# Kernel optimization log

Hardware: AMD Instinct MI355X
Metric: run time of the kernel (lower is better)

Reference implementation:

```python
import jax, jax.numpy as jnp
import numpy as np

EPS_ROW = 1e-8
EPS_BN = 1e-5


def _row_norm(A):
    # A / clamp(rowsum, 1e-8)
    return A / jnp.clip(A.sum(axis=1, keepdims=True), EPS_ROW, None)


def _bn_eval(x, gamma, beta, mean, var):
    return (x - mean) * (gamma / jnp.sqrt(var + EPS_BN)) + beta


def setup_inputs() -> dict:
    key = jax.random.key(0)
    ks = jax.random.split(key, 12)
    n_src, n_tgt = 8192, 16384
    d_src, d_tgt_in, d_hid, d_out = 256, 128, 128, 64

    def xavier(k, fan_in, fan_out):
        lim = float(np.sqrt(6.0 / (fan_in + fan_out)))
        # stored as [in, out] so forward is x @ W + b
        return jax.random.uniform(k, (fan_in, fan_out), jnp.float32, -lim, lim)

    inp = {
        "H_source": jax.random.normal(ks[0], (n_src, d_src), jnp.float32),
        "H_target": jax.random.normal(ks[1], (n_tgt, d_tgt_in), jnp.float32),
        "A": jax.random.uniform(ks[2], (n_tgt, n_src), jnp.float32),
        "W0": xavier(ks[3], d_src, d_hid),
        "b0": jnp.zeros((d_hid,), jnp.float32),
        "Wb0": xavier(ks[4], d_hid, d_hid),
        "bb0": jnp.zeros((d_hid,), jnp.float32),
        "W1": xavier(ks[5], d_hid, d_hid),
        "b1": jnp.zeros((d_hid,), jnp.float32),
        # fwd BN layers (i=0 and i=2): stacked [2, d_hid]
        "bn_f_gamma": jax.random.uniform(ks[6], (2, d_hid), jnp.float32, 0.5, 1.5),
        "bn_f_beta": jax.random.normal(ks[7], (2, d_hid), jnp.float32) * 0.1,
        "bn_f_mean": jax.random.normal(ks[8], (2, d_hid), jnp.float32) * 0.1,
        "bn_f_var": jax.random.uniform(ks[9], (2, d_hid), jnp.float32, 0.5, 1.5),
        # bwd BN layer (i=1)
        "bn_b_gamma": jax.random.uniform(ks[10], (d_hid,), jnp.float32, 0.5, 1.5),
        "bn_b_beta": jnp.zeros((d_hid,), jnp.float32),
        "bn_b_mean": jnp.zeros((d_hid,), jnp.float32),
        "bn_b_var": jnp.ones((d_hid,), jnp.float32),
        "Wout": xavier(ks[11], d_hid, d_out),
        "bout": jnp.zeros((d_out,), jnp.float32),
    }
    return inp


def reference(H_source, H_target, A, W0, b0, Wb0, bb0, W1, b1,
              bn_f_gamma, bn_f_beta, bn_f_mean, bn_f_var,
              bn_b_gamma, bn_b_beta, bn_b_mean, bn_b_var,
              Wout, bout):
    # Inference mode: dropout = identity, BatchNorm uses running stats.
    A_n = _row_norm(A)          # [n_tgt, n_src]
    AT_n = _row_norm(A.T)       # [n_src, n_tgt]

    # layer 0 (fwd): target <- source
    h_tgt = (A_n @ H_source) @ W0 + b0
    h_tgt = jax.nn.relu(_bn_eval(h_tgt, bn_f_gamma[0], bn_f_beta[0], bn_f_mean[0], bn_f_var[0]))

    # layer 1 (bwd): source <- target
    h_src = (AT_n @ h_tgt) @ Wb0 + bb0
    h_src = jax.nn.relu(_bn_eval(h_src, bn_b_gamma, bn_b_beta, bn_b_mean, bn_b_var))

    # layer 2 (fwd): target <- source
    h_tgt = (A_n @ h_src) @ W1 + b1
    h_tgt = jax.nn.relu(_bn_eval(h_tgt, bn_f_gamma[1], bn_f_beta[1], bn_f_mean[1], bn_f_var[1]))

    return h_tgt @ Wout + bout  # [n_tgt, d_out]
```

## Files before the change

### kernel.cpp

```cpp
#include <hip/hip_runtime.h>
#include <hip/hip_bf16.h>
#include <stdint.h>

typedef unsigned short ushort_t;
typedef float   f32x4  __attribute__((ext_vector_type(4)));
typedef short   bf16x8 __attribute__((ext_vector_type(8)));

#define NSRC 8192
#define NTGT 16384

__device__ __forceinline__ ushort_t f2bf(float f){
  union { float f; uint32_t u; } v; v.f = f;
  uint32_t r = v.u + 0x7fffu + ((v.u >> 16) & 1u);
  return (ushort_t)(r >> 16);
}
__device__ __forceinline__ uint2 pack4(f32x4 v){
  uint2 r;
  r.x = (uint32_t)f2bf(v.x) | ((uint32_t)f2bf(v.y) << 16);
  r.y = (uint32_t)f2bf(v.z) | ((uint32_t)f2bf(v.w) << 16);
  return r;
}
__device__ __forceinline__ bf16x8 cvt8(f32x4 lo, f32x4 hi){
  union { uint4 u; bf16x8 h; } x;
  uint2 a = pack4(lo), b = pack4(hi);
  x.u = make_uint4(a.x, a.y, b.x, b.y);
  return x.h;
}
__device__ __forceinline__ uint4 asu4(bf16x8 v){ union { bf16x8 h; uint4 u; } x; x.h = v; return x.u; }
__device__ __forceinline__ float sum4(f32x4 v){ return v.x + v.y + v.z + v.w; }

typedef __attribute__((address_space(1))) const uint32_t* gas_t;
typedef __attribute__((address_space(3))) uint32_t* las_t;
__device__ __forceinline__ void dma16(const void* g, void* l){
  __builtin_amdgcn_global_load_lds((gas_t)g, (las_t)l, 16, 0, 0);
}

__global__ __launch_bounds__(256) void k_wt(const float* __restrict__ S, ushort_t* __restrict__ D,
                                            int R, int C){
  __shared__ float tile[32][33];
  const int cb = blockIdx.x * 32, rb = blockIdx.y * 32;
  const int tx = threadIdx.x & 31, ty = threadIdx.x >> 5;
#pragma unroll
  for (int i = 0; i < 4; ++i)
    tile[ty + 8*i][tx] = S[(size_t)(rb + ty + 8*i) * C + cb + tx];
  __syncthreads();
#pragma unroll
  for (int i = 0; i < 4; ++i)
    D[(size_t)(cb + ty + 8*i) * R + rb + tx] = f2bf(tile[tx][ty + 8*i]);
}

__global__ __launch_bounds__(256) void k_packH(const float* __restrict__ S, ushort_t* __restrict__ D){
  int u = blockIdx.x * 4 + (threadIdx.x >> 6);
  int lane = threadIdx.x & 63;
  int nb = u >> 8, kb = u & 255;
  int fr = lane & 15, q = lane >> 4;
  ushort_t buf[8];
#pragma unroll
  for (int j = 0; j < 8; ++j)
    buf[j] = f2bf(S[(size_t)(kb * 32 + q * 8 + j) * 256 + nb * 16 + fr]);
  *(uint4*)&D[((size_t)nb * 256 + kb) * 512 + (size_t)lane * 8] = *(uint4*)buf;
}

__global__ void k_init_b2p_tail(ushort_t* __restrict__ B2p){
  int idx = blockIdx.x * 256 + threadIdx.x;
  int lane = idx & 63;
  int kb = idx >> 6;
  int fr = lane & 15;
  uint32_t v = (fr == 0) ? 0x3F803F80u : 0u;
  uint4 val = {v, v, v, v};
  *(uint4*)&B2p[((size_t)8 * 512 + kb) * 512 + (size_t)lane * 8] = val;
}

__global__ __launch_bounds__(256) void k_gemm1(const float* __restrict__ A,
    const ushort_t* __restrict__ B1p, float* __restrict__ P2, float* __restrict__ rowsumP,
    ushort_t* __restrict__ Abf){
  __shared__ ushort_t Bls[2][16 * 512];
  const int t = threadIdx.x;
  const int mb = blockIdx.x, kc = blockIdx.y;
  const size_t m0 = (size_t)mb * 64;
  const int k0 = kc * 2048;
  const int kb0 = k0 >> 5;

  const int w = t >> 6, lane = t & 63;
  const int wr = w >> 1, wc = w & 1;
  const int fr = lane & 15, q = lane >> 4;

  const float* pa0 = &A[(m0 + wr * 32 + fr) * (size_t)NSRC + k0 + q * 8];
  const float* pa1 = pa0 + (size_t)16 * NSRC;
  ushort_t* pw0 = &Abf[(m0 + wr * 32 + fr) * (size_t)NSRC + k0 + q * 8];
  ushort_t* pw1 = pw0 + (size_t)16 * NSRC;

#pragma unroll
  for (int i = 0; i < 4; ++i){
    int f = w * 4 + i;
    dma16(&B1p[((size_t)f * 256 + kb0) * 512 + (size_t)lane * 8], &Bls[0][f * 512]);
  }
  f32x4 c0a = *(const f32x4*)pa0, c0b = *(const f32x4*)(pa0 + 4);
  f32x4 c1a = *(const f32x4*)pa1, c1b = *(const f32x4*)(pa1 + 4);

  f32x4 acc[2][8];
  const f32x4 vz = {0.f, 0.f, 0.f, 0.f};
#pragma unroll
  for (int i = 0; i < 2; ++i)
#pragma unroll
    for (int j = 0; j < 8; ++j) acc[i][j] = vz;
  float rs0 = 0.f, rs1 = 0.f;
  __syncthreads();

  for (int kt = 0; kt < 64; ++kt){
    const int cur = kt & 1;
    f32x4 n0a, n0b, n1a, n1b;
    if (kt < 63){
#pragma unroll
      for (int i = 0; i < 4; ++i){
        int f = w * 4 + i;
        dma16(&B1p[((size_t)f * 256 + kb0 + kt + 1) * 512 + (size_t)lane * 8],
              &Bls[cur ^ 1][f * 512]);
      }
      n0a = *(const f32x4*)(pa0 + (kt + 1) * 32);
      n0b = *(const f32x4*)(pa0 + (kt + 1) * 32 + 4);
      n1a = *(const f32x4*)(pa1 + (kt + 1) * 32);
      n1b = *(const f32x4*)(pa1 + (kt + 1) * 32 + 4);
    }

    rs0 += sum4(c0a) + sum4(c0b);
    rs1 += sum4(c1a) + sum4(c1b);
    bf16x8 af0 = cvt8(c0a, c0b);
    bf16x8 af1 = cvt8(c1a, c1b);
    if (wc == 0){
      *(uint4*)&pw0[kt * 32] = asu4(af0);
      *(uint4*)&pw1[kt * 32] = asu4(af1);
    }
#pragma unroll
    for (int fn = 0; fn < 8; ++fn){
      bf16x8 bfv = *(bf16x8*)&Bls[cur][(wc * 8 + fn) * 512 + lane * 8];
      acc[0][fn] = __builtin_amdgcn_mfma_f32_16x16x32_bf16(af0, bfv, acc[0][fn], 0, 0, 0);
      acc[1][fn] = __builtin_amdgcn_mfma_f32_16x16x32_bf16(af1, bfv, acc[1][fn], 0, 0, 0);
    }
    if (kt < 63){ c0a = n0a; c0b = n0b; c1a = n1a; c1b = n1b; }
    __syncthreads();
  }

  float* Pd = P2 + (size_t)kc * NTGT * 256;
#pragma unroll
  for (int fm = 0; fm < 2; ++fm)
#pragma unroll
    for (int j = 0; j < 4; ++j){
      int row = wr * 32 + fm * 16 + q * 4 + j;
#pragma unroll
      for (int fn = 0; fn < 8; ++fn)
        Pd[(m0 + row) * 256 + wc * 128 + fn * 16 + fr] = acc[fm][fn][j];
    }

  rs0 += __shfl_xor(rs0, 16); rs0 += __shfl_xor(rs0, 32);
  rs1 += __shfl_xor(rs1, 16); rs1 += __shfl_xor(rs1, 32);
  if (wc == 0 && q == 0){
    rowsumP[(size_t)kc * NTGT + m0 + wr * 32 + fr]      = rs0;
    rowsumP[(size_t)kc * NTGT + m0 + wr * 32 + 16 + fr] = rs1;
  }
}

__global__ __launch_bounds__(256) void k_gemm2(const ushort_t* __restrict__ Abf,
    const ushort_t* __restrict__ B2p, float* __restrict__ G2p){
  __shared__ ushort_t Bls[2][9 * 512];
  const int t = threadIdx.x;
  const int sb = blockIdx.x, kc = blockIdx.y;
  const size_t s0 = (size_t)sb * 64;
  const int k0 = kc * 2048;
  const int kb0 = k0 >> 5;

  const int w = t >> 6, lane = t & 63;
  const int fr = lane & 15, q = lane >> 4;
  const size_t scol = s0 + w * 16 + fr;
  const ushort_t* pA = &Abf[(size_t)(k0 + q * 8) * NSRC + scol];

  const int f0 = w * 3;
  const int nf = (w < 3) ? 3 : 0;

#pragma unroll
  for (int i = 0; i < 3; ++i){
    if (i < nf)
      dma16(&B2p[((size_t)(f0 + i) * 512 + kb0) * 512 + (size_t)lane * 8], &Bls[0][(f0 + i) * 512]);
  }
  ushort_t arc[8];
#pragma unroll
  for (int j = 0; j < 8; ++j)
    arc[j] = pA[(size_t)j * NSRC];

  f32x4 acc[9];
  const f32x4 vz = {0.f, 0.f, 0.f, 0.f};
#pragma unroll
  for (int j = 0; j < 9; ++j) acc[j] = vz;
  __syncthreads();

  for (int kt = 0; kt < 64; ++kt){
    const int cur = kt & 1;
    ushort_t arn[8];
    if (kt < 63){
#pragma unroll
      for (int i = 0; i < 3; ++i){
        if (i < nf)
          dma16(&B2p[((size_t)(f0 + i) * 512 + kb0 + kt + 1) * 512 + (size_t)lane * 8],
                &Bls[cur ^ 1][(f0 + i) * 512]);
      }
#pragma unroll
      for (int j = 0; j < 8; ++j)
        arn[j] = pA[((size_t)(kt + 1) * 32 + j) * NSRC];
    }

    bf16x8 af;
#pragma unroll
    for (int j = 0; j < 8; ++j) af[j] = (short)arc[j];
#pragma unroll
    for (int fn = 0; fn < 9; ++fn){
      bf16x8 bfv = *(bf16x8*)&Bls[cur][fn * 512 + lane * 8];
      acc[fn] = __builtin_amdgcn_mfma_f32_16x16x32_bf16(af, bfv, acc[fn], 0, 0, 0);
    }
    if (kt < 63){
#pragma unroll
      for (int j = 0; j < 8; ++j) arc[j] = arn[j];
    }
    __syncthreads();
  }

  float* Pd = G2p + (size_t)kc * NSRC * 144;
#pragma unroll
  for (int j = 0; j < 4; ++j){
    int row = w * 16 + q * 4 + j;
#pragma unroll
    for (int fn = 0; fn < 9; ++fn)
      Pd[(s0 + row) * 144 + fn * 16 + fr] = acc[fn][j];
  }
}

__global__ __launch_bounds__(256) void k_gemm3(const ushort_t* __restrict__ Abf,
    const ushort_t* __restrict__ B3p, float* __restrict__ G3p){
  __shared__ ushort_t Bls[2][8 * 512];
  const int t = threadIdx.x;
  const int mb = blockIdx.x, kc = blockIdx.y;
  const size_t m0 = (size_t)mb * 64;
  const int k0 = kc * 2048;
  const int kb0 = k0 >> 5;

  const int w = t >> 6, lane = t & 63;
  const int wr = w >> 1, wc = w & 1;
  const int fr = lane & 15, q = lane >> 4;

  const ushort_t* pa0 = &Abf[(m0 + wr * 32 + fr) * (size_t)NSRC + k0 + q * 8];
  const ushort_t* pa1 = pa0 + (size_t)16 * NSRC;

#pragma unroll
  for (int i = 0; i < 2; ++i){
    int f = w * 2 + i;
    dma16(&B3p[((size_t)f * 256 + kb0) * 512 + (size_t)lane * 8], &Bls[0][f * 512]);
  }
  bf16x8 a0c = *(const bf16x8*)pa0;
  bf16x8 a1c = *(const bf16x8*)pa1;

  f32x4 acc[2][4];
  const f32x4 vz = {0.f, 0.f, 0.f, 0.f};
#pragma unroll
  for (int i = 0; i < 2; ++i)
#pragma unroll
    for (int j = 0; j < 4; ++j) acc[i][j] = vz;
  __syncthreads();

  for (int kt = 0; kt < 64; ++kt){
    const int cur = kt & 1;
    bf16x8 a0n, a1n;
    if (kt < 63){
#pragma unroll
      for (int i = 0; i < 2; ++i){
        int f = w * 2 + i;
        dma16(&B3p[((size_t)f * 256 + kb0 + kt + 1) * 512 + (size_t)lane * 8],
              &Bls[cur ^ 1][f * 512]);
      }
      a0n = *(const bf16x8*)(pa0 + (kt + 1) * 32);
      a1n = *(const bf16x8*)(pa1 + (kt + 1) * 32);
    }

#pragma unroll
    for (int fn = 0; fn < 4; ++fn){
      bf16x8 bfv = *(bf16x8*)&Bls[cur][(wc * 4 + fn) * 512 + lane * 8];
      acc[0][fn] = __builtin_amdgcn_mfma_f32_16x16x32_bf16(a0c, bfv, acc[0][fn], 0, 0, 0);
      acc[1][fn] = __builtin_amdgcn_mfma_f32_16x16x32_bf16(a1c, bfv, acc[1][fn], 0, 0, 0);
    }
    if (kt < 63){ a0c = a0n; a1c = a1n; }
    __syncthreads();
  }

  float* Pd = G3p + (size_t)kc * NTGT * 128;
#pragma unroll
  for (int fm = 0; fm < 2; ++fm)
#pragma unroll
    for (int j = 0; j < 4; ++j){
      int row = wr * 32 + fm * 16 + q * 4 + j;
#pragma unroll
      for (int fn = 0; fn < 4; ++fn)
        Pd[(m0 + row) * 128 + wc * 64 + fn * 16 + fr] = acc[fm][fn][j];
    }
}

__global__ __launch_bounds__(256) void k_s1(
    const float* __restrict__ P2, const float* __restrict__ rowsumP,
    const ushort_t* __restrict__ W0t, const float* __restrict__ b0,
    const float* __restrict__ g, const float* __restrict__ be,
    const float* __restrict__ mu, const float* __restrict__ va,
    ushort_t* __restrict__ B2p)
{
  __shared__ ushort_t Xs[64 * 72];
  __shared__ ushort_t Ws[128 * 72];
  __shared__ float    os[64 * 132];
  __shared__ float invs[64], scs[128], mbs[128];
  const int t = threadIdx.x;
  const size_t m0 = (size_t)blockIdx.x * 64;
  const size_t CH = (size_t)NTGT * 256;

  if (t < 64){
    float rsv = rowsumP[m0 + t] + rowsumP[(size_t)NTGT + m0 + t]
              + rowsumP[2 * (size_t)NTGT + m0 + t] + rowsumP[3 * (size_t)NTGT + m0 + t];
    invs[t] = 1.0f / fmaxf(rsv, 1e-8f);
  } else if (t < 192){
    int n = t - 64;
    float s = g[n] * rsqrtf(va[n] + 1e-5f);
    scs[n] = s;
    mbs[n] = (b0[n] - mu[n]) * s + be[n];
  }
  __syncthreads();

  const int w = t >> 6, lane = t & 63;
  const int wr = w >> 1, wc = w & 1;
  const int fr = lane & 15, q = lane >> 4;
  f32x4 acc[2][4];
  const f32x4 vz = {0.f, 0.f, 0.f, 0.f};
#pragma unroll
  for (int i = 0; i < 2; ++i)
#pragma unroll
    for (int j = 0; j < 4; ++j) acc[i][j] = vz;

  for (int kt = 0; kt < 4; ++kt){
    const int kk = kt * 64;
    __syncthreads();
#pragma unroll
    for (int r = 0; r < 4; ++r){
      int c = t + 256 * r;
      int row = c >> 4, col4 = (c & 15) * 4;
      const float* pa = &P2[(m0 + row) * 256 + kk + col4];
      f32x4 v0 = *(const f32x4*)pa;
      f32x4 v1 = *(const f32x4*)(pa + CH);
      f32x4 v2 = *(const f32x4*)(pa + 2 * CH);
      f32x4 v3 = *(const f32x4*)(pa + 3 * CH);
      f32x4 v = (v0 + v1 + v2 + v3) * invs[row];
      *(uint2*)&Xs[row * 72 + col4] = pack4(v);
    }
#pragma unroll
    for (int r = 0; r < 4; ++r){
      int c = t + 256 * r;
      int n = c >> 3, k8 = (c & 7) * 8;
      *(uint4*)&Ws[n * 72 + k8] = *(const uint4*)&W0t[(size_t)n * 256 + kk + k8];
    }
    __syncthreads();
#pragma unroll
    for (int ks = 0; ks < 2; ++ks){
      bf16x8 af[2], bfv[4];
      af[0] = *(const bf16x8*)&Xs[(wr * 32 + fr) * 72 + ks * 32 + q * 8];
      af[1] = *(const bf16x8*)&Xs[(wr * 32 + 16 + fr) * 72 + ks * 32 + q * 8];
#pragma unroll
      for (int fn = 0; fn < 4; ++fn)
        bfv[fn] = *(const bf16x8*)&Ws[(wc * 64 + fn * 16 + fr) * 72 + ks * 32 + q * 8];
#pragma unroll
      for (int fm = 0; fm < 2; ++fm)
#pragma unroll
        for (int fn = 0; fn < 4; ++fn)
          acc[fm][fn] = __builtin_amdgcn_mfma_f32_16x16x32_bf16(af[fm], bfv[fn], acc[fm][fn], 0, 0, 0);
    }
  }

#pragma unroll
  for (int fm = 0; fm < 2; ++fm)
#pragma unroll
    for (int fn = 0; fn < 4; ++fn){
      int n = wc * 64 + fn * 16 + fr;
      float s = scs[n], mb = mbs[n];
#pragma unroll
      for (int j = 0; j < 4; ++j){
        int row = wr * 32 + fm * 16 + q * 4 + j;
        os[row * 132 + n] = fmaxf(acc[fm][fn][j] * s + mb, 0.f);
      }
    }
  __syncthreads();
  {
    const int kb0 = (int)(m0 >> 5);
#pragma unroll
    for (int r = 0; r < 4; ++r){
      int s = t + 256 * r;
      int lane2 = s & 63;
      int kb2 = (s >> 6) & 1;
      int nb = s >> 7;
      int fr2 = lane2 & 15, q2 = lane2 >> 4;
      int n = nb * 16 + fr2;
      ushort_t buf[8];
#pragma unroll
      for (int j = 0; j < 8; ++j)
        buf[j] = f2bf(os[(kb2 * 32 + q2 * 8 + j) * 132 + n]);
      *(uint4*)&B2p[((size_t)nb * 512 + kb0 + kb2) * 512 + (size_t)lane2 * 8] = *(uint4*)buf;
    }
  }
}

__global__ __launch_bounds__(256) void k_s2(
    const float* __restrict__ G2p,
    const ushort_t* __restrict__ Wb0t, const float* __restrict__ bb0,
    const float* __restrict__ g, const float* __restrict__ be,
    const float* __restrict__ mu, const float* __restrict__ va,
    ushort_t* __restrict__ B3p)
{
  __shared__ ushort_t Xs[64 * 72];
  __shared__ ushort_t Ws[128 * 72];
  __shared__ float    os[64 * 132];
  __shared__ float invs[64], scs[128], mbs[128];
  const int t = threadIdx.x;
  const size_t m0 = (size_t)blockIdx.x * 64;
  const size_t CH = (size_t)NSRC * 144;

  if (t < 64){
    size_t row = m0 + t;
    float c = 0.f;
#pragma unroll
    for (int i = 0; i < 8; ++i) c += G2p[i * CH + row * 144 + 128];
    invs[t] = 1.0f / fmaxf(c, 1e-8f);
  } else if (t < 192){
    int n = t - 64;
    float s = g[n] * rsqrtf(va[n] + 1e-5f);
    scs[n] = s;
    mbs[n] = (bb0[n] - mu[n]) * s + be[n];
  }
  __syncthreads();

  const int w = t >> 6, lane = t & 63;
  const int wr = w >> 1, wc = w & 1;
  const int fr = lane & 15, q = lane >> 4;
  f32x4 acc[2][4];
  const f32x4 vz = {0.f, 0.f, 0.f, 0.f};
#pragma unroll
  for (int i = 0; i < 2; ++i)
#pragma unroll
    for (int j = 0; j < 4; ++j) acc[i][j] = vz;

  for (int kt = 0; kt < 2; ++kt){
    const int kk = kt * 64;
    __syncthreads();
#pragma unroll
    for (int r = 0; r < 4; ++r){
      int c = t + 256 * r;
      int row = c >> 4, col4 = (c & 15) * 4;
      const float* pa = &G2p[(m0 + row) * 144 + kk + col4];
      f32x4 v = {0.f, 0.f, 0.f, 0.f};
#pragma unroll
      for (int i = 0; i < 8; ++i) v += *(const f32x4*)(pa + i * CH);
      v *= invs[row];
      *(uint2*)&Xs[row * 72 + col4] = pack4(v);
    }
#pragma unroll
    for (int r = 0; r < 4; ++r){
      int c = t + 256 * r;
      int n = c >> 3, k8 = (c & 7) * 8;
      *(uint4*)&Ws[n * 72 + k8] = *(const uint4*)&Wb0t[(size_t)n * 128 + kk + k8];
    }
    __syncthreads();
#pragma unroll
    for (int ks = 0; ks < 2; ++ks){
      bf16x8 af[2], bfv[4];
      af[0] = *(const bf16x8*)&Xs[(wr * 32 + fr) * 72 + ks * 32 + q * 8];
      af[1] = *(const bf16x8*)&Xs[(wr * 32 + 16 + fr) * 72 + ks * 32 + q * 8];
#pragma unroll
      for (int fn = 0; fn < 4; ++fn)
        bfv[fn] = *(const bf16x8*)&Ws[(wc * 64 + fn * 16 + fr) * 72 + ks * 32 + q * 8];
#pragma unroll
      for (int fm = 0; fm < 2; ++fm)
#pragma unroll
        for (int fn = 0; fn < 4; ++fn)
          acc[fm][fn] = __builtin_amdgcn_mfma_f32_16x16x32_bf16(af[fm], bfv[fn], acc[fm][fn], 0, 0, 0);
    }
  }

#pragma unroll
  for (int fm = 0; fm < 2; ++fm)
#pragma unroll
    for (int fn = 0; fn < 4; ++fn){
      int n = wc * 64 + fn * 16 + fr;
      float s = scs[n], mb = mbs[n];
#pragma unroll
      for (int j = 0; j < 4; ++j){
        int row = wr * 32 + fm * 16 + q * 4 + j;
        os[row * 132 + n] = fmaxf(acc[fm][fn][j] * s + mb, 0.f);
      }
    }
  __syncthreads();
  {
    const int kb0 = (int)(m0 >> 5);
#pragma unroll
    for (int r = 0; r < 4; ++r){
      int s = t + 256 * r;
      int lane2 = s & 63;
      int kb2 = (s >> 6) & 1;
      int nb = s >> 7;
      int fr2 = lane2 & 15, q2 = lane2 >> 4;
      int n = nb * 16 + fr2;
      ushort_t buf[8];
#pragma unroll
      for (int j = 0; j < 8; ++j)
        buf[j] = f2bf(os[(kb2 * 32 + q2 * 8 + j) * 132 + n]);
      *(uint4*)&B3p[((size_t)nb * 256 + kb0 + kb2) * 512 + (size_t)lane2 * 8] = *(uint4*)buf;
    }
  }
}

__global__ __launch_bounds__(256) void k_s3(
    const float* __restrict__ G3p, const float* __restrict__ rowsumP,
    const ushort_t* __restrict__ W1t, const float* __restrict__ b1,
    const float* __restrict__ g, const float* __restrict__ be,
    const float* __restrict__ mu, const float* __restrict__ va,
    const ushort_t* __restrict__ Woutt, const float* __restrict__ bout,
    float* __restrict__ out)
{
  __shared__ ushort_t Xs[64 * 72];
  __shared__ ushort_t Ws[128 * 72];
  __shared__ ushort_t ys[64 * 136];
  __shared__ ushort_t Ws2[64 * 136];
  __shared__ float invs[64], scs[128], mbs[128];
  const int t = threadIdx.x;
  const size_t m0 = (size_t)blockIdx.x * 64;
  const size_t CH = (size_t)NTGT * 128;

  if (t < 64){
    float rsv = rowsumP[m0 + t] + rowsumP[(size_t)NTGT + m0 + t]
              + rowsumP[2 * (size_t)NTGT + m0 + t] + rowsumP[3 * (size_t)NTGT + m0 + t];
    invs[t] = 1.0f / fmaxf(rsv, 1e-8f);
  } else if (t < 192){
    int n = t - 64;
    float s = g[n] * rsqrtf(va[n] + 1e-5f);
    scs[n] = s;
    mbs[n] = (b1[n] - mu[n]) * s + be[n];
  }
#pragma unroll
  for (int r = 0; r < 4; ++r){
    int c = t + 256 * r;
    int n = c >> 4, k8 = (c & 15) * 8;
    *(uint4*)&Ws2[n * 136 + k8] = *(const uint4*)&Woutt[(size_t)n * 128 + k8];
  }
  __syncthreads();

  const int w = t >> 6, lane = t & 63;
  const int wr = w >> 1, wc = w & 1;
  const int fr = lane & 15, q = lane >> 4;
  f32x4 acc[2][4];
  const f32x4 vz = {0.f, 0.f, 0.f, 0.f};
#pragma unroll
  for (int i = 0; i < 2; ++i)
#pragma unroll
    for (int j = 0; j < 4; ++j) acc[i][j] = vz;

  for (int kt = 0; kt < 2; ++kt){
    const int kk = kt * 64;
    __syncthreads();
#pragma unroll
    for (int r = 0; r < 4; ++r){
      int c = t + 256 * r;
      int row = c >> 4, col4 = (c & 15) * 4;
      const float* pa = &G3p[(m0 + row) * 128 + kk + col4];
      f32x4 v0 = *(const f32x4*)pa;
      f32x4 v1 = *(const f32x4*)(pa + CH);
      f32x4 v2 = *(const f32x4*)(pa + 2 * CH);
      f32x4 v3 = *(const f32x4*)(pa + 3 * CH);
      f32x4 v = (v0 + v1 + v2 + v3) * invs[row];
      *(uint2*)&Xs[row * 72 + col4] = pack4(v);
    }
#pragma unroll
    for (int r = 0; r < 4; ++r){
      int c = t + 256 * r;
      int n = c >> 3, k8 = (c & 7) * 8;
      *(uint4*)&Ws[n * 72 + k8] = *(const uint4*)&W1t[(size_t)n * 128 + kk + k8];
    }
    __syncthreads();
#pragma unroll
    for (int ks = 0; ks < 2; ++ks){
      bf16x8 af[2], bfv[4];
      af[0] = *(const bf16x8*)&Xs[(wr * 32 + fr) * 72 + ks * 32 + q * 8];
      af[1] = *(const bf16x8*)&Xs[(wr * 32 + 16 + fr) * 72 + ks * 32 + q * 8];
#pragma unroll
      for (int fn = 0; fn < 4; ++fn)
        bfv[fn] = *(const bf16x8*)&Ws[(wc * 64 + fn * 16 + fr) * 72 + ks * 32 + q * 8];
#pragma unroll
      for (int fm = 0; fm < 2; ++fm)
#pragma unroll
        for (int fn = 0; fn < 4; ++fn)
          acc[fm][fn] = __builtin_amdgcn_mfma_f32_16x16x32_bf16(af[fm], bfv[fn], acc[fm][fn], 0, 0, 0);
    }
  }

#pragma unroll
  for (int fm = 0; fm < 2; ++fm)
#pragma unroll
    for (int fn = 0; fn < 4; ++fn){
      int n = wc * 64 + fn * 16 + fr;
      float s = scs[n], mb = mbs[n];
#pragma unroll
      for (int j = 0; j < 4; ++j){
        int row = wr * 32 + fm * 16 + q * 4 + j;
        ys[row * 136 + n] = f2bf(fmaxf(acc[fm][fn][j] * s + mb, 0.f));
      }
    }
  __syncthreads();

  f32x4 acc2[2][2];
#pragma unroll
  for (int i = 0; i < 2; ++i)
#pragma unroll
    for (int j = 0; j < 2; ++j) acc2[i][j] = vz;
#pragma unroll
  for (int ks = 0; ks < 4; ++ks){
    bf16x8 af[2], bfv[2];
    af[0] = *(const bf16x8*)&ys[(wr * 32 + fr) * 136 + ks * 32 + q * 8];
    af[1] = *(const bf16x8*)&ys[(wr * 32 + 16 + fr) * 136 + ks * 32 + q * 8];
#pragma unroll
    for (int fn = 0; fn < 2; ++fn)
      bfv[fn] = *(const bf16x8*)&Ws2[(wc * 32 + fn * 16 + fr) * 136 + ks * 32 + q * 8];
#pragma unroll
    for (int fm = 0; fm < 2; ++fm)
#pragma unroll
      for (int fn = 0; fn < 2; ++fn)
        acc2[fm][fn] = __builtin_amdgcn_mfma_f32_16x16x32_bf16(af[fm], bfv[fn], acc2[fm][fn], 0, 0, 0);
  }
#pragma unroll
  for (int fm = 0; fm < 2; ++fm)
#pragma unroll
    for (int fn = 0; fn < 2; ++fn){
      int n = wc * 32 + fn * 16 + fr;
      float bo = bout[n];
#pragma unroll
      for (int j = 0; j < 4; ++j){
        int row = wr * 32 + fm * 16 + q * 4 + j;
        out[(m0 + row) * 64 + n] = acc2[fm][fn][j] + bo;
      }
    }
}

extern "C" void kernel_launch(void* const* d_in, const int* in_sizes, int n_in,
                              void* d_out, int out_size, void* d_ws, size_t ws_size,
                              hipStream_t stream) {
  const float* Hs  = (const float*)d_in[0];
  const float* A   = (const float*)d_in[2];
  const float* W0  = (const float*)d_in[3];
  const float* b0  = (const float*)d_in[4];
  const float* Wb0 = (const float*)d_in[5];
  const float* bb0 = (const float*)d_in[6];
  const float* W1  = (const float*)d_in[7];
  const float* b1  = (const float*)d_in[8];
  const float* bnfg= (const float*)d_in[9];
  const float* bnfb= (const float*)d_in[10];
  const float* bnfm= (const float*)d_in[11];
  const float* bnfv= (const float*)d_in[12];
  const float* bnbg= (const float*)d_in[13];
  const float* bnbb= (const float*)d_in[14];
  const float* bnbm= (const float*)d_in[15];
  const float* bnbv= (const float*)d_in[16];
  const float* Wout= (const float*)d_in[17];
  const float* bout= (const float*)d_in[18];
  float* out = (float*)d_out;

  char* ws = (char*)d_ws;
  float*    R1    = (float*)ws;
  constexpr size_t OFF_ABF  = 67108864;
  constexpr size_t OFF_B1P  = OFF_ABF + 268435456;
  constexpr size_t OFF_B2P  = OFF_B1P + 4194304;
  constexpr size_t OFF_B3P  = OFF_B2P + 4718592;
  constexpr size_t OFF_RS   = OFF_B3P + 2097152;
  constexpr size_t OFF_W0T  = OFF_RS  + 262144;
  constexpr size_t OFF_WB0T = OFF_W0T + 65536;
  constexpr size_t OFF_W1T  = OFF_WB0T + 32768;
  constexpr size_t OFF_WOT  = OFF_W1T + 32768;
  ushort_t* Abf  = (ushort_t*)(ws + OFF_ABF);
  ushort_t* B1p  = (ushort_t*)(ws + OFF_B1P);
  ushort_t* B2p  = (ushort_t*)(ws + OFF_B2P);
  ushort_t* B3p  = (ushort_t*)(ws + OFF_B3P);
  float*    rsP  = (float*)   (ws + OFF_RS);
  ushort_t* W0t  = (ushort_t*)(ws + OFF_W0T);
  ushort_t* Wb0t = (ushort_t*)(ws + OFF_WB0T);
  ushort_t* W1t  = (ushort_t*)(ws + OFF_W1T);
  ushort_t* Wott = (ushort_t*)(ws + OFF_WOT);

  k_packH<<<1024, 256, 0, stream>>>(Hs, B1p);
  k_wt<<<dim3(128/32, 256/32),  256, 0, stream>>>(W0,  W0t, 256, 128);
  k_wt<<<dim3(128/32, 128/32),  256, 0, stream>>>(Wb0, Wb0t, 128, 128);
  k_wt<<<dim3(128/32, 128/32),  256, 0, stream>>>(W1,  W1t, 128, 128);
  k_wt<<<dim3(64/32, 128/32),   256, 0, stream>>>(Wout, Wott, 128, 64);
  k_init_b2p_tail<<<128, 256, 0, stream>>>(B2p);

  k_gemm1<<<dim3(256, 4), 256, 0, stream>>>(A, B1p, R1, rsP, Abf);
  k_s1<<<256, 256, 0, stream>>>(R1, rsP, W0t, b0, bnfg, bnfb, bnfm, bnfv, B2p);
  k_gemm2<<<dim3(128, 8), 256, 0, stream>>>(Abf, B2p, R1);
  k_s2<<<128, 256, 0, stream>>>(R1, Wb0t, bb0, bnbg, bnbb, bnbm, bnbv, B3p);
  k_gemm3<<<dim3(256, 4), 256, 0, stream>>>(Abf, B3p, R1);
  k_s3<<<256, 256, 0, stream>>>(R1, rsP, W1t, b1, bnfg + 128, bnfb + 128, bnfm + 128, bnfv + 128,
                                Wott, bout, out);
}
```

Baseline: 553.6 us.

## Deepen A-operand prefetch to two stages with partial vmcnt waits in GEMM kernels

In the three GEMM kernels, register prefetch of the A operand goes from one k-step ahead to two, and __syncthreads is replaced by explicit s_waitcnt vmcnt(N) plus s_barrier, with sched_barrier fences fixing instruction order. The goal is to keep more global loads in flight so the loop no longer drains all memory operations every iteration. GEMM1 also splits the bf16 writeback so each wave column stores one row-half, and GEMM2 spreads B DMA across all four waves. The hand-counted vmcnt values are fragile: a miscount gives a race or an over-wait, and the extra prefetch registers raise register pressure.

```diff
diff --git a/kernel.cpp b/kernel.cpp
--- a/kernel.cpp
+++ b/kernel.cpp
@@ -34,6 +34,7 @@
 __device__ __forceinline__ void dma16(const void* g, void* l){
   __builtin_amdgcn_global_load_lds((gas_t)g, (las_t)l, 16, 0, 0);
 }
+#define SCHED_FENCE() __builtin_amdgcn_sched_barrier(0)
 
 __global__ __launch_bounds__(256) void k_wt(const float* __restrict__ S, ushort_t* __restrict__ D,
                                             int R, int C){
@@ -89,27 +90,37 @@
   const float* pa1 = pa0 + (size_t)16 * NSRC;
   ushort_t* pw0 = &Abf[(m0 + wr * 32 + fr) * (size_t)NSRC + k0 + q * 8];
   ushort_t* pw1 = pw0 + (size_t)16 * NSRC;
+  ushort_t* pw  = (wc == 0) ? pw0 : pw1;
+
+  f32x4 acc[2][8];
+  const f32x4 vz = {0.f, 0.f, 0.f, 0.f};
+#pragma unroll
+  for (int i = 0; i < 2; ++i)
+#pragma unroll
+    for (int j = 0; j < 8; ++j) acc[i][j] = vz;
+  float rs0 = 0.f, rs1 = 0.f;
 
 #pragma unroll
   for (int i = 0; i < 4; ++i){
     int f = w * 4 + i;
     dma16(&B1p[((size_t)f * 256 + kb0) * 512 + (size_t)lane * 8], &Bls[0][f * 512]);
   }
-  f32x4 c0a = *(const f32x4*)pa0, c0b = *(const f32x4*)(pa0 + 4);
-  f32x4 c1a = *(const f32x4*)pa1, c1b = *(const f32x4*)(pa1 + 4);
-
-  f32x4 acc[2][8];
-  const f32x4 vz = {0.f, 0.f, 0.f, 0.f};
-#pragma unroll
-  for (int i = 0; i < 2; ++i)
-#pragma unroll
-    for (int j = 0; j < 8; ++j) acc[i][j] = vz;
-  float rs0 = 0.f, rs1 = 0.f;
-  __syncthreads();
+  SCHED_FENCE();
+  f32x4 c0a = *(const f32x4*)pa0,        c0b = *(const f32x4*)(pa0 + 4);
+  f32x4 c1a = *(const f32x4*)pa1,        c1b = *(const f32x4*)(pa1 + 4);
+  f32x4 d0a = *(const f32x4*)(pa0 + 32), d0b = *(const f32x4*)(pa0 + 36);
+  f32x4 d1a = *(const f32x4*)(pa1 + 32), d1b = *(const f32x4*)(pa1 + 36);
+  asm volatile("s_waitcnt vmcnt(8)" ::: "memory");
+  SCHED_FENCE();
+  __builtin_amdgcn_s_barrier();
 
   for (int kt = 0; kt < 64; ++kt){
     const int cur = kt & 1;
-    f32x4 n0a, n0b, n1a, n1b;
+    rs0 += sum4(c0a) + sum4(c0b);
+    rs1 += sum4(c1a) + sum4(c1b);
+    bf16x8 af0 = cvt8(c0a, c0b);
+    bf16x8 af1 = cvt8(c1a, c1b);
+
     if (kt < 63){
 #pragma unroll
       for (int i = 0; i < 4; ++i){
@@ -117,28 +128,24 @@
         dma16(&B1p[((size_t)f * 256 + kb0 + kt + 1) * 512 + (size_t)lane * 8],
               &Bls[cur ^ 1][f * 512]);
       }
-      n0a = *(const f32x4*)(pa0 + (kt + 1) * 32);
-      n0b = *(const f32x4*)(pa0 + (kt + 1) * 32 + 4);
-      n1a = *(const f32x4*)(pa1 + (kt + 1) * 32);
-      n1b = *(const f32x4*)(pa1 + (kt + 1) * 32 + 4);
-    }
-
-    rs0 += sum4(c0a) + sum4(c0b);
-    rs1 += sum4(c1a) + sum4(c1b);
-    bf16x8 af0 = cvt8(c0a, c0b);
-    bf16x8 af1 = cvt8(c1a, c1b);
-    if (wc == 0){
-      *(uint4*)&pw0[kt * 32] = asu4(af0);
-      *(uint4*)&pw1[kt * 32] = asu4(af1);
-    }
+    }
+    SCHED_FENCE();
+    c0a = d0a; c0b = d0b; c1a = d1a; c1b = d1b;
+    if (kt < 62){
+      d0a = *(const f32x4*)(pa0 + (kt + 2) * 32); d0b = *(const f32x4*)(pa0 + (kt + 2) * 32 + 4);
+      d1a = *(const f32x4*)(pa1 + (kt + 2) * 32); d1b = *(const f32x4*)(pa1 + (kt + 2) * 32 + 4);
+    }
+    *(uint4*)&pw[kt * 32] = asu4(wc == 0 ? af0 : af1);
+
 #pragma unroll
     for (int fn = 0; fn < 8; ++fn){
       bf16x8 bfv = *(bf16x8*)&Bls[cur][(wc * 8 + fn) * 512 + lane * 8];
       acc[0][fn] = __builtin_amdgcn_mfma_f32_16x16x32_bf16(af0, bfv, acc[0][fn], 0, 0, 0);
       acc[1][fn] = __builtin_amdgcn_mfma_f32_16x16x32_bf16(af1, bfv, acc[1][fn], 0, 0, 0);
     }
-    if (kt < 63){ c0a = n0a; c0b = n0b; c1a = n1a; c1b = n1b; }
-    __syncthreads();
+    asm volatile("s_waitcnt vmcnt(5)" ::: "memory");
+    SCHED_FENCE();
+    __builtin_amdgcn_s_barrier();
   }
 
   float* Pd = P2 + (size_t)kc * NTGT * 256;
@@ -174,53 +181,59 @@
   const size_t scol = s0 + w * 16 + fr;
   const ushort_t* pA = &Abf[(size_t)(k0 + q * 8) * NSRC + scol];
 
-  const int f0 = w * 3;
-  const int nf = (w < 3) ? 3 : 0;
-
-#pragma unroll
-  for (int i = 0; i < 3; ++i){
-    if (i < nf)
-      dma16(&B2p[((size_t)(f0 + i) * 512 + kb0) * 512 + (size_t)lane * 8], &Bls[0][(f0 + i) * 512]);
-  }
-  ushort_t arc[8];
-#pragma unroll
-  for (int j = 0; j < 8; ++j)
-    arc[j] = pA[(size_t)j * NSRC];
-
   f32x4 acc[9];
   const f32x4 vz = {0.f, 0.f, 0.f, 0.f};
 #pragma unroll
   for (int j = 0; j < 9; ++j) acc[j] = vz;
-  __syncthreads();
+
+#pragma unroll
+  for (int i = 0; i < 3; ++i){
+    int f = w + i * 4;
+    if (f < 9)
+      dma16(&B2p[((size_t)f * 512 + kb0) * 512 + (size_t)lane * 8], &Bls[0][f * 512]);
+  }
+  SCHED_FENCE();
+  ushort_t aN[8], aX[8];
+#pragma unroll
+  for (int j = 0; j < 8; ++j) aN[j] = pA[(size_t)j * NSRC];
+#pragma unroll
+  for (int j = 0; j < 8; ++j) aX[j] = pA[(size_t)(32 + j) * NSRC];
+  asm volatile("s_waitcnt vmcnt(16)" ::: "memory");
+  SCHED_FENCE();
+  __builtin_amdgcn_s_barrier();
 
   for (int kt = 0; kt < 64; ++kt){
     const int cur = kt & 1;
-    ushort_t arn[8];
+    bf16x8 af;
+#pragma unroll
+    for (int j = 0; j < 8; ++j) af[j] = (short)aN[j];
+
     if (kt < 63){
 #pragma unroll
       for (int i = 0; i < 3; ++i){
-        if (i < nf)
-          dma16(&B2p[((size_t)(f0 + i) * 512 + kb0 + kt + 1) * 512 + (size_t)lane * 8],
-                &Bls[cur ^ 1][(f0 + i) * 512]);
+        int f = w + i * 4;
+        if (f < 9)
+          dma16(&B2p[((size_t)f * 512 + kb0 + kt + 1) * 512 + (size_t)lane * 8],
+                &Bls[cur ^ 1][f * 512]);
       }
+    }
+    SCHED_FENCE();
+#pragma unroll
+    for (int j = 0; j < 8; ++j) aN[j] = aX[j];
+    if (kt < 62){
 #pragma unroll
       for (int j = 0; j < 8; ++j)
-        arn[j] = pA[((size_t)(kt + 1) * 32 + j) * NSRC];
-    }
-
-    bf16x8 af;
-#pragma unroll
-    for (int j = 0; j < 8; ++j) af[j] = (short)arc[j];
+        aX[j] = pA[((size_t)(kt + 2) * 32 + j) * NSRC];
+    }
+
 #pragma unroll
     for (int fn = 0; fn < 9; ++fn){
       bf16x8 bfv = *(bf16x8*)&Bls[cur][fn * 512 + lane * 8];
       acc[fn] = __builtin_amdgcn_mfma_f32_16x16x32_bf16(af, bfv, acc[fn], 0, 0, 0);
     }
-    if (kt < 63){
-#pragma unroll
-      for (int j = 0; j < 8; ++j) arc[j] = arn[j];
-    }
-    __syncthreads();
+    asm volatile("s_waitcnt vmcnt(8)" ::: "memory");
+    SCHED_FENCE();
+    __builtin_amdgcn_s_barrier();
   }
 
   float* Pd = G2p + (size_t)kc * NSRC * 144;
@@ -249,25 +262,31 @@
   const ushort_t* pa0 = &Abf[(m0 + wr * 32 + fr) * (size_t)NSRC + k0 + q * 8];
   const ushort_t* pa1 = pa0 + (size_t)16 * NSRC;
 
+  f32x4 acc[2][4];
+  const f32x4 vz = {0.f, 0.f, 0.f, 0.f};
+#pragma unroll
+  for (int i = 0; i < 2; ++i)
+#pragma unroll
+    for (int j = 0; j < 4; ++j) acc[i][j] = vz;
+
 #pragma unroll
   for (int i = 0; i < 2; ++i){
     int f = w * 2 + i;
     dma16(&B3p[((size_t)f * 256 + kb0) * 512 + (size_t)lane * 8], &Bls[0][f * 512]);
   }
-  bf16x8 a0c = *(const bf16x8*)pa0;
-  bf16x8 a1c = *(const bf16x8*)pa1;
-
-  f32x4 acc[2][4];
-  const f32x4 vz = {0.f, 0.f, 0.f, 0.f};
-#pragma unroll
-  for (int i = 0; i < 2; ++i)
-#pragma unroll
-    for (int j = 0; j < 4; ++j) acc[i][j] = vz;
-  __syncthreads();
+  SCHED_FENCE();
+  bf16x8 a0N = *(const bf16x8*)pa0;
+  bf16x8 a1N = *(const bf16x8*)pa1;
+  bf16x8 a0X = *(const bf16x8*)(pa0 + 32);
+  bf16x8 a1X = *(const bf16x8*)(pa1 + 32);
+  asm volatile("s_waitcnt vmcnt(4)" ::: "memory");
+  SCHED_FENCE();
+  __builtin_amdgcn_s_barrier();
 
   for (int kt = 0; kt < 64; ++kt){
     const int cur = kt & 1;
-    bf16x8 a0n, a1n;
+    bf16x8 u0 = a0N, u1 = a1N;
+
     if (kt < 63){
 #pragma unroll
       for (int i = 0; i < 2; ++i){
@@ -275,18 +294,23 @@
         dma16(&B3p[((size_t)f * 256 + kb0 + kt + 1) * 512 + (size_t)lane * 8],
               &Bls[cur ^ 1][f * 512]);
       }
-      a0n = *(const bf16x8*)(pa0 + (kt + 1) * 32);
-      a1n = *(const bf16x8*)(pa1 + (kt + 1) * 32);
+    }
+    SCHED_FENCE();
+    a0N = a0X; a1N = a1X;
+    if (kt < 62){
+      a0X = *(const bf16x8*)(pa0 + (kt + 2) * 32);
+      a1X = *(const bf16x8*)(pa1 + (kt + 2) * 32);
     }
 
 #pragma unroll
     for (int fn = 0; fn < 4; ++fn){
       bf16x8 bfv = *(bf16x8*)&Bls[cur][(wc * 4 + fn) * 512 + lane * 8];
-      acc[0][fn] = __builtin_amdgcn_mfma_f32_16x16x32_bf16(a0c, bfv, acc[0][fn], 0, 0, 0);
-      acc[1][fn] = __builtin_amdgcn_mfma_f32_16x16x32_bf16(a1c, bfv, acc[1][fn], 0, 0, 0);
-    }
-    if (kt < 63){ a0c = a0n; a1c = a1n; }
-    __syncthreads();
+      acc[0][fn] = __builtin_amdgcn_mfma_f32_16x16x32_bf16(u0, bfv, acc[0][fn], 0, 0, 0);
+      acc[1][fn] = __builtin_amdgcn_mfma_f32_16x16x32_bf16(u1, bfv, acc[1][fn], 0, 0, 0);
+    }
+    asm volatile("s_waitcnt vmcnt(2)" ::: "memory");
+    SCHED_FENCE();
+    __builtin_amdgcn_s_barrier();
   }
 
   float* Pd = G3p + (size_t)kc * NTGT * 128;
```

After: 558.8 us. No clear change (+0.9%).
